# Performance work log

Measured on AMD Instinct MI355X. Metric: run time of the kernel, lower is better.

The kernel has to match this reference:

```python
import jax, jax.numpy as jnp
import numpy as np

HID = 128; H = 8; D = HID // H; L = 2; IN = 128; OUT = 32
ND = 20000; NF = 50000; E = 400000
SQRT_D = float(np.sqrt(D))
LN_EPS = 1e-5


def setup_inputs() -> dict:
    key = jax.random.key(0)
    ks = jax.random.split(key, 16)
    s = 1.0 / np.sqrt(HID)
    n = lambda k, sh, sc=1.0: jax.random.normal(k, sh, jnp.float32) * sc
    return dict(
        x_device=n(ks[0], (ND, IN)),
        x_feature=n(ks[1], (NF, IN)),
        e_df_src=jax.random.randint(ks[2], (E,), 0, ND),
        e_df_dst=jax.random.randint(ks[3], (E,), 0, NF),
        e_fd_src=jax.random.randint(ks[4], (E,), 0, NF),
        e_fd_dst=jax.random.randint(ks[5], (E,), 0, ND),
        W_dev_in=n(ks[6], (IN, HID), s), b_dev_in=jnp.zeros((HID,), jnp.float32),
        W_feat_in=n(ks[7], (IN, HID), s), b_feat_in=jnp.zeros((HID,), jnp.float32),
        Wk=n(ks[8], (L, 2, HID, HID), s), bk=jnp.zeros((L, 2, HID), jnp.float32),
        Wq=n(ks[9], (L, 2, HID, HID), s), bq=jnp.zeros((L, 2, HID), jnp.float32),
        Wv=n(ks[10], (L, 2, HID, HID), s), bv=jnp.zeros((L, 2, HID), jnp.float32),
        a_rel=n(ks[11], (L, 2, H, D, D), 1.0 / np.sqrt(D)),
        m_rel=n(ks[12], (L, 2, H, D, D), 1.0 / np.sqrt(D)),
        p_rel=jnp.ones((L, 2, H), jnp.float32),
        Wa=n(ks[13], (L, 2, HID, HID), s), ba=jnp.zeros((L, 2, HID), jnp.float32),
        skip=jnp.ones((L, 2), jnp.float32),
        ln_g=jnp.ones((L, 2, HID), jnp.float32), ln_b=jnp.zeros((L, 2, HID), jnp.float32),
        W_out=n(ks[14], (HID, OUT), s), b_out=jnp.zeros((OUT,), jnp.float32),
    )


def _layer_norm(x, g, b):
    m = x.mean(-1, keepdims=True)
    v = ((x - m) ** 2).mean(-1, keepdims=True)
    return (x - m) * jax.lax.rsqrt(v + LN_EPS) * g + b


def _edge_agg(q_dst, k_src, v_src, a_r, m_r, p_r, src, dst, n_dst):
    # per-edge-type relation transforms of source k/v: [N_src,H,D]
    kt = jnp.einsum('nhd,hde->nhe', k_src, a_r)
    vt = jnp.einsum('nhd,hde->nhe', v_src, m_r)
    # per-edge attention logits [E,H], scaled by relation prior
    logit = (q_dst[dst] * kt[src]).sum(-1) * p_r / SQRT_D
    # segment softmax over incoming edges of each dst node (per edge type)
    mx = jax.ops.segment_max(logit, dst, num_segments=n_dst)
    ex = jnp.exp(logit - mx[dst])
    sm = jax.ops.segment_sum(ex, dst, num_segments=n_dst)
    alpha = ex / (sm[dst] + 1e-16)
    # attention-weighted message scatter-sum -> [n_dst,H,D]
    return jax.ops.segment_sum(vt[src] * alpha[..., None], dst, num_segments=n_dst)


def _forward(x_device, x_feature, W_dev_in, b_dev_in, W_feat_in, b_feat_in,
             Wk, bk, Wq, bq, Wv, bv, a_rel, m_rel, p_rel, Wa, ba, skip,
             ln_g, ln_b, W_out, b_out, e_df_src, e_df_dst, e_fd_src, e_fd_dst):
    x_d = jax.nn.relu(x_device @ W_dev_in + b_dev_in)
    x_f = jax.nn.relu(x_feature @ W_feat_in + b_feat_in)
    for l in range(L):
        xs = (x_d, x_f)  # node-type 0 = device, 1 = feature
        k = [(xs[t] @ Wk[l, t] + bk[l, t]).reshape(-1, H, D) for t in range(2)]
        q = [(xs[t] @ Wq[l, t] + bq[l, t]).reshape(-1, H, D) for t in range(2)]
        v = [(xs[t] @ Wv[l, t] + bv[l, t]).reshape(-1, H, D) for t in range(2)]
        # edge type 0: device -> feature ; edge type 1: feature -> device
        agg_f = _edge_agg(q[1], k[0], v[0], a_rel[l, 0], m_rel[l, 0], p_rel[l, 0],
                          e_df_src, e_df_dst, NF)
        agg_d = _edge_agg(q[0], k[1], v[1], a_rel[l, 1], m_rel[l, 1], p_rel[l, 1],
                          e_fd_src, e_fd_dst, ND)
        new = []
        for t, agg in ((0, agg_d), (1, agg_f)):
            o = jax.nn.gelu(agg.reshape(-1, HID), approximate=False) @ Wa[l, t] + ba[l, t]
            sk = jax.nn.sigmoid(skip[l, t])
            o = sk * o + (1.0 - sk) * xs[t]              # HGTConv skip
            new.append(_layer_norm(xs[t] + o, ln_g[l, t], ln_b[l, t]))  # wrapper residual+LN (dropout=identity in eval)
        x_d, x_f = new
    return x_d @ W_out + b_out


def reference(x_device, x_feature, e_df_src, e_df_dst, e_fd_src, e_fd_dst,
              W_dev_in, b_dev_in, W_feat_in, b_feat_in, Wk, bk, Wq, bq, Wv, bv,
              a_rel, m_rel, p_rel, Wa, ba, skip, ln_g, ln_b, W_out, b_out):
    return _forward(x_device, x_feature, W_dev_in, b_dev_in, W_feat_in, b_feat_in,
                    Wk, bk, Wq, bq, Wv, bv, a_rel, m_rel, p_rel, Wa, ba, skip,
                    ln_g, ln_b, W_out, b_out, e_df_src, e_df_dst, e_fd_src, e_fd_dst)
```

## Files before the change

kernel.cpp:

```cpp
#include <hip/hip_runtime.h>
#include <math.h>

#define ND 20000
#define NF 50000
#define NE 400000
#define NT (NF + ND)
#define NBKT 256
#define BKTW 274

typedef __attribute__((ext_vector_type(8))) short short8;
typedef __attribute__((ext_vector_type(4))) float f32x4;
typedef __attribute__((ext_vector_type(2))) float f32x2;
typedef unsigned short us;
typedef unsigned char u8;

static __device__ __forceinline__ us f2bf(float f) {
    unsigned u = __builtin_bit_cast(unsigned, f);
    u += 0x7FFF + ((u >> 16) & 1);
    return (us)(u >> 16);
}
static __device__ __forceinline__ float bf2f(us h) {
    return __builtin_bit_cast(float, (unsigned)h << 16);
}
static __device__ __forceinline__ float bflo(unsigned u) {
    return __builtin_bit_cast(float, u << 16);
}
static __device__ __forceinline__ float bfhi(unsigned u) {
    return __builtin_bit_cast(float, u & 0xFFFF0000u);
}
static __device__ __forceinline__ float gelu_f(float x) {
    return 0.5f * x * (1.0f + erff(x * 0.70710678118654752f));
}

static __device__ __forceinline__ u8 f2fp8(float f) {
    unsigned u = __builtin_bit_cast(unsigned, f);
    unsigned s = (u >> 24) & 0x80u;
    unsigned a = u & 0x7FFFFFFFu;
    if (a >= 0x43E00000u) return (u8)(s | 0x7Eu);
    if (a < 0x3C800000u) {
        float af = __builtin_bit_cast(float, a);
        unsigned q = (unsigned)(af * 512.0f + 0.5f);
        return (u8)(s | q);
    }
    unsigned r = a + 0x7FFFFu + ((a >> 20) & 1u);
    unsigned e8 = (r >> 23) - 120u;
    unsigned m3 = (r >> 20) & 7u;
    return (u8)(s | (e8 << 3) | m3);
}

__global__ void k_hist_prep(const int* __restrict__ dA, const int* __restrict__ dB,
                            int* __restrict__ blockhist, int HB,
                            const float* __restrict__ W_dev_in, const float* __restrict__ W_feat_in,
                            const float* __restrict__ Wq, const float* __restrict__ Wk,
                            const float* __restrict__ Wv, const float* __restrict__ Wa,
                            const float* __restrict__ b_dev_in, const float* __restrict__ b_feat_in,
                            const float* __restrict__ bq, const float* __restrict__ bk,
                            const float* __restrict__ bv, const float* __restrict__ ba,
                            const float* __restrict__ a_rel, const float* __restrict__ m_rel,
                            const float* __restrict__ p_rel,
                            us* __restrict__ WT, float* __restrict__ B_all) {
    __shared__ int hist[NBKT];
    if ((int)blockIdx.x < HB) {
        hist[threadIdx.x] = 0;
        __syncthreads();
        int base_e = blockIdx.x * 4096;
        #pragma unroll
        for (int j = 0; j < 16; ++j) {
            int e = base_e + j * 256 + threadIdx.x;
            if (e < 2 * NE) {
                int g = (e < NE) ? dA[e] : (NF + dB[e - NE]);
                atomicAdd(&hist[g / BKTW], 1);
            }
        }
        __syncthreads();
        blockhist[blockIdx.x * NBKT + threadIdx.x] = hist[threadIdx.x];
        return;
    }
    int idx = (blockIdx.x - HB) * 256 + threadIdx.x;
    if (idx < 18 * 16384) {
        int k = idx & 127, c = (idx >> 7) & 127, id = idx >> 14;
        float val;
        if (id == 0) val = W_dev_in[k * 128 + c];
        else if (id == 1) val = W_feat_in[k * 128 + c];
        else if (id < 6) val = Wq[(id - 2) * 16384 + k * 128 + c];
        else if (id < 10) {
            int lt = id - 6, h = c >> 4, e = c & 15;
            const float* A = a_rel + (lt * 8 + h) * 256;
            const float* Ws = Wk + lt * 16384 + k * 128 + h * 16;
            float sm = 0.f;
            #pragma unroll
            for (int d = 0; d < 16; ++d) sm += Ws[d] * A[d * 16 + e];
            val = sm * p_rel[lt * 8 + h] * 0.25f;
        } else if (id < 14) {
            int lt = id - 10, h = c >> 4, e = c & 15;
            const float* A = m_rel + (lt * 8 + h) * 256;
            const float* Ws = Wv + lt * 16384 + k * 128 + h * 16;
            float sm = 0.f;
            #pragma unroll
            for (int d = 0; d < 16; ++d) sm += Ws[d] * A[d * 16 + e];
            val = sm;
        } else val = Wa[(id - 14) * 16384 + k * 128 + c];
        WT[(size_t)id * 16384 + (((c * 128 + k)) ^ ((c & 7) << 3))] = f2bf(val);
    } else {
        int j = idx - 18 * 16384;
        if (j >= 18 * 128) return;
        int c = j & 127, id = j >> 7;
        float v;
        if (id == 0) v = b_dev_in[c];
        else if (id == 1) v = b_feat_in[c];
        else if (id < 6) v = bq[(id - 2) * 128 + c];
        else if (id < 10) {
            int lt = id - 6, h = c >> 4, e = c & 15;
            const float* A = a_rel + (lt * 8 + h) * 256;
            const float* bs = bk + lt * 128 + h * 16;
            float sm = 0.f;
            #pragma unroll
            for (int d = 0; d < 16; ++d) sm += bs[d] * A[d * 16 + e];
            v = sm * p_rel[lt * 8 + h] * 0.25f;
        } else if (id < 14) {
            int lt = id - 10, h = c >> 4, e = c & 15;
            const float* A = m_rel + (lt * 8 + h) * 256;
            const float* bs = bv + lt * 128 + h * 16;
            float sm = 0.f;
            #pragma unroll
            for (int d = 0; d < 16; ++d) sm += bs[d] * A[d * 16 + e];
            v = sm;
        } else v = ba[(id - 14) * 128 + c];
        B_all[j] = v;
    }
}

__global__ void k_scanA(int* __restrict__ blockhist, int* __restrict__ totals, int HB) {
    __shared__ int sd[256];
    int b = blockIdx.x, t = threadIdx.x;
    int v = (t < HB) ? blockhist[t * NBKT + b] : 0;
    sd[t] = v; __syncthreads();
    for (int off = 1; off < 256; off <<= 1) {
        int add = (t >= off) ? sd[t - off] : 0;
        __syncthreads();
        sd[t] += add;
        __syncthreads();
    }
    if (t < HB) blockhist[t * NBKT + b] = sd[t] - v;
    if (t == 255) totals[b] = sd[255];
}

__global__ void k_scatter(const int* __restrict__ sA, const int* __restrict__ dA,
                          const int* __restrict__ sB, const int* __restrict__ dB,
                          const int* __restrict__ blockhist, const int* __restrict__ totals,
                          uint2* __restrict__ pairs) {
    __shared__ int lcur[NBKT];
    __shared__ int sdb[NBKT];
    int t = threadIdx.x;
    int tv = totals[t];
    sdb[t] = tv; __syncthreads();
    for (int off = 1; off < 256; off <<= 1) {
        int add = (t >= off) ? sdb[t - off] : 0;
        __syncthreads();
        sdb[t] += add;
        __syncthreads();
    }
    lcur[t] = (sdb[t] - tv) + blockhist[blockIdx.x * NBKT + t];
    __syncthreads();
    int base_e = blockIdx.x * 4096;
    #pragma unroll
    for (int j = 0; j < 16; ++j) {
        int e = base_e + j * 256 + t;
        if (e < 2 * NE) {
            int src, g;
            if (e < NE) { src = sA[e]; g = dA[e]; }
            else        { src = sB[e - NE]; g = NF + dB[e - NE]; }
            int pos = atomicAdd(&lcur[g / BKTW], 1);
            pairs[pos] = make_uint2((unsigned)src, (unsigned)g);
        }
    }
}

__global__ void k_bucket_csr(const uint2* __restrict__ pairs, const int* __restrict__ totals,
                             int* __restrict__ rs, int* __restrict__ esrc) {
    __shared__ int cnt[BKTW];
    __shared__ int excl[BKTW];
    __shared__ int sdb[NBKT];
    __shared__ int sde[NBKT];
    int b = blockIdx.x, t = threadIdx.x;
    int tv = totals[t];
    sdb[t] = tv; __syncthreads();
    for (int off = 1; off < 256; off <<= 1) {
        int add = (t >= off) ? sdb[t - off] : 0;
        __syncthreads();
        sdb[t] += add;
        __syncthreads();
    }
    sde[t] = sdb[t] - tv;
    __syncthreads();
    int start = sde[b], end = sdb[b];
    int g0 = b * BKTW;
    for (int i = t; i < BKTW; i += 256) cnt[i] = 0;
    __syncthreads();
    for (int i = start + t; i < end; i += 256)
        atomicAdd(&cnt[(int)pairs[i].y - g0], 1);
    __syncthreads();
    if (t < 64) {
        int lane = t;
        int vals[5]; int s = 0;
        #pragma unroll
        for (int j = 0; j < 5; ++j) {
            int i = lane * 5 + j;
            vals[j] = (i < BKTW) ? cnt[i] : 0;
            s += vals[j];
        }
        int incl = s;
        #pragma unroll
        for (int off = 1; off < 64; off <<= 1) {
            int n = __shfl_up(incl, off);
            if (lane >= off) incl += n;
        }
        int run = incl - s;
        #pragma unroll
        for (int j = 0; j < 5; ++j) {
            int i = lane * 5 + j;
            if (i < BKTW) excl[i] = run;
            run += vals[j];
        }
    }
    __syncthreads();
    int nloc = min(BKTW, NT - g0);
    for (int i = t; i < nloc; i += 256) rs[g0 + i] = start + excl[i];
    if (b == NBKT - 1 && t == 0) rs[NT] = sdb[255];
    __syncthreads();
    for (int i = start + t; i < end; i += 256) {
        uint2 p = pairs[i];
        int pos = start + atomicAdd(&excl[(int)p.y - g0], 1);
        esrc[pos] = (int)p.x;
    }
}

template<int MODE, int AF32, int RELU>
__global__ __launch_bounds__(256) void mfma_gemm2(
    const void* __restrict__ X0, const void* __restrict__ X1,
    const us* __restrict__ WT0, const float* __restrict__ Ball,
    us* __restrict__ Y0, us* __restrict__ Y1,
    int N0, int N1, int GB0, int widbase,
    us* __restrict__ K0, us* __restrict__ K1,
    u8* __restrict__ V0, u8* __restrict__ V1,
    const float* __restrict__ skipv, const float* __restrict__ lng,
    const float* __restrict__ lnb) {
    __shared__ us Wlds[16384];
    const int type = (blockIdx.x >= (unsigned)GB0) ? 1 : 0;
    const int bx = blockIdx.x - (type ? GB0 : 0);
    const int N = type ? N1 : N0;
    const void* Xv = type ? X1 : X0;
    const int NP = (MODE == 1) ? 3 : 1;

    const int lane = threadIdx.x & 63;
    const int wave = threadIdx.x >> 6;
    const int row_base = bx * 128 + wave * 32;
    const int l15 = lane & 15, lg = lane >> 4;
    const int kbase = lg * 8;

    {
        const char* gsrc = (const char*)(WT0 + (size_t)(widbase + type) * 16384)
                           + wave * 8192 + lane * 16;
        char* ldst = (char*)Wlds + wave * 8192;
        #pragma unroll
        for (int i = 0; i < 8; ++i) {
            __builtin_amdgcn_global_load_lds(
                (const __attribute__((address_space(1))) void*)(gsrc + i * 1024),
                (__attribute__((address_space(3))) void*)(ldst + i * 1024),
                16, 0, 0);
        }
    }

    short8 a[2][4];
    #pragma unroll
    for (int mf = 0; mf < 2; ++mf) {
        int r = row_base + mf * 16 + l15;
        r = r < N ? r : N - 1;
        if (AF32) {
            const float* Xf = (const float*)Xv + (size_t)r * 128;
            #pragma unroll
            for (int kf = 0; kf < 4; ++kf) {
                float4 lo = *(const float4*)(Xf + kf * 32 + kbase);
                float4 hi = *(const float4*)(Xf + kf * 32 + kbase + 4);
                short8 t;
                t[0] = (short)f2bf(lo.x); t[1] = (short)f2bf(lo.y);
                t[2] = (short)f2bf(lo.z); t[3] = (short)f2bf(lo.w);
                t[4] = (short)f2bf(hi.x); t[5] = (short)f2bf(hi.y);
                t[6] = (short)f2bf(hi.z); t[7] = (short)f2bf(hi.w);
                a[mf][kf] = t;
            }
        } else {
            const us* Xb = (const us*)Xv + (size_t)r * 128;
            #pragma unroll
            for (int kf = 0; kf < 4; ++kf)
                a[mf][kf] = *(const short8*)(Xb + kf * 32 + kbase);
        }
    }

    __syncthreads();

    const unsigned swz = (unsigned)((l15 & 7) << 4);

    for (int p = 0; p < NP; ++p) {
        const int wid = widbase + type + 4 * p;
        const float* bias = Ball + wid * 128;

        f32x4 acc[2][8];
        #pragma unroll
        for (int mf = 0; mf < 2; ++mf)
            #pragma unroll
            for (int cf = 0; cf < 8; ++cf) acc[mf][cf] = (f32x4){0.f, 0.f, 0.f, 0.f};

        #pragma unroll
        for (int cf = 0; cf < 8; ++cf) {
            const unsigned rowbyte = (unsigned)((cf * 16 + l15) * 256 + kbase * 2);
            #pragma unroll
            for (int kf = 0; kf < 4; ++kf) {
                short8 b = *(const short8*)((const char*)Wlds + ((rowbyte + kf * 64) ^ swz));
                acc[0][cf] = __builtin_amdgcn_mfma_f32_16x16x32_bf16(a[0][kf], b, acc[0][cf], 0, 0, 0);
                acc[1][cf] = __builtin_amdgcn_mfma_f32_16x16x32_bf16(a[1][kf], b, acc[1][cf], 0, 0, 0);
            }
        }

        if (MODE == 1 && p + 1 < NP) {
            __syncthreads();
            const char* gsrc = (const char*)(WT0 + (size_t)(widbase + type + 4 * (p + 1)) * 16384)
                               + wave * 8192 + lane * 16;
            char* ldst = (char*)Wlds + wave * 8192;
            #pragma unroll
            for (int i = 0; i < 8; ++i) {
                __builtin_amdgcn_global_load_lds(
                    (const __attribute__((address_space(1))) void*)(gsrc + i * 1024),
                    (__attribute__((address_space(3))) void*)(ldst + i * 1024),
                    16, 0, 0);
            }
        }

        float bval[8];
        #pragma unroll
        for (int cf = 0; cf < 8; ++cf) bval[cf] = bias[cf * 16 + l15];

        if (MODE == 2) {
            const int lt = widbase - 14 + type;
            float sk = 1.f / (1.f + __expf(-skipv[lt]));
            float gv[8], bv2[8];
            #pragma unroll
            for (int cf = 0; cf < 8; ++cf) {
                gv[cf]  = lng[(size_t)lt * 128 + cf * 16 + l15];
                bv2[cf] = lnb[(size_t)lt * 128 + cf * 16 + l15];
            }
            us* xw = type ? K1 : K0;
            #pragma unroll
            for (int mf = 0; mf < 2; ++mf)
                #pragma unroll
                for (int r = 0; r < 4; ++r) {
                    int grow = row_base + mf * 16 + lg * 4 + r;
                    if (grow >= N) continue;
                    float t[8];
                    float sum = 0.f;
                    #pragma unroll
                    for (int cf = 0; cf < 8; ++cf) {
                        float o = acc[mf][cf][r] + bval[cf];
                        float x = bf2f(xw[(size_t)grow * 128 + cf * 16 + l15]);
                        t[cf] = (2.f - sk) * x + sk * o;
                        sum += t[cf];
                    }
                    sum += __shfl_xor(sum, 1); sum += __shfl_xor(sum, 2);
                    sum += __shfl_xor(sum, 4); sum += __shfl_xor(sum, 8);
                    float mean = sum * (1.0f / 128.0f);
                    float vs = 0.f;
                    #pragma unroll
                    for (int cf = 0; cf < 8; ++cf) { t[cf] -= mean; vs += t[cf] * t[cf]; }
                    vs += __shfl_xor(vs, 1); vs += __shfl_xor(vs, 2);
                    vs += __shfl_xor(vs, 4); vs += __shfl_xor(vs, 8);
                    float inv = rsqrtf(vs * (1.0f / 128.0f) + 1e-5f);
                    #pragma unroll
                    for (int cf = 0; cf < 8; ++cf)
                        xw[(size_t)grow * 128 + cf * 16 + l15] = f2bf(t[cf] * inv * gv[cf] + bv2[cf]);
                }
        } else {
            #pragma unroll
            for (int mf = 0; mf < 2; ++mf)
                #pragma unroll
                for (int r = 0; r < 4; ++r) {
                    int grow = row_base + mf * 16 + lg * 4 + r;
                    if (grow >= N) continue;
                    #pragma unroll
                    for (int cf = 0; cf < 8; ++cf) {
                        float v = acc[mf][cf][r] + bval[cf];
                        if (RELU) v = fmaxf(v, 0.f);
                        int col = cf * 16 + l15;
                        if (MODE == 0 || p == 0) {
                            (type ? Y1 : Y0)[(size_t)grow * 128 + col] = f2bf(v);
                        } else if (p == 1) {
                            (type ? K1 : K0)[(size_t)grow * 128 + col] = f2bf(v);
                        } else {
                            (type ? V1 : V0)[(size_t)grow * 128 + col] = f2fp8(v);
                        }
                    }
                }
        }

        if (MODE == 1 && p + 1 < NP) __syncthreads();
    }
}

__global__ __launch_bounds__(256) void gemm_out_k(
    const us* __restrict__ X, const float* __restrict__ W,
    const float* __restrict__ bias, float* __restrict__ Y, int N) {
    __shared__ float Ws[128 * 32];
    __shared__ float Xs[8][128];
    const int tid = threadIdx.x;
    const int row0 = blockIdx.x * 8;
    #pragma unroll
    for (int it = 0; it < 16; ++it) Ws[it * 256 + tid] = W[it * 256 + tid];
    #pragma unroll
    for (int it = 0; it < 2; ++it) {
        int idx = it * 256 + tid;
        int rr = idx >> 6, kp = idx & 63;
        int gr = row0 + rr;
        unsigned u = (gr < N) ? *(const unsigned*)(X + (size_t)gr * 128 + kp * 2) : 0u;
        Xs[rr][kp * 2]     = bflo(u);
        Xs[rr][kp * 2 + 1] = bfhi(u);
    }
    __syncthreads();
    const int rr = tid >> 5, c = tid & 31;
    float acc = bias[c];
    #pragma unroll 8
    for (int k = 0; k < 128; ++k)
        acc = fmaf(Xs[rr][k], Ws[k * 32 + c], acc);
    int gr = row0 + rr;
    if (gr < N) Y[(size_t)gr * 32 + c] = acc;
}

#define EDGE_STEP(kc, vc, pidx)                                        \
    {                                                                  \
        float part = qv[0] * bflo(kc.x);                               \
        part = fmaf(qv[1], bfhi(kc.x), part);                          \
        part = fmaf(qv[2], bflo(kc.y), part);                          \
        part = fmaf(qv[3], bfhi(kc.y), part);                          \
        part = fmaf(qv[4], bflo(kc.z), part);                          \
        part = fmaf(qv[5], bfhi(kc.z), part);                          \
        part = fmaf(qv[6], bflo(kc.w), part);                          \
        part = fmaf(qv[7], bfhi(kc.w), part);                          \
        part += __shfl_xor(part, 1);                                   \
        float w = ((pidx) < p1) ? __expf(part) : 0.f;                  \
        s += w;                                                        \
        f32x2 v01 = __builtin_amdgcn_cvt_pk_f32_fp8((int)vc.x, false); \
        f32x2 v23 = __builtin_amdgcn_cvt_pk_f32_fp8((int)vc.x, true);  \
        f32x2 v45 = __builtin_amdgcn_cvt_pk_f32_fp8((int)vc.y, false); \
        f32x2 v67 = __builtin_amdgcn_cvt_pk_f32_fp8((int)vc.y, true);  \
        a[0] = fmaf(w, v01.x, a[0]);                                   \
        a[1] = fmaf(w, v01.y, a[1]);                                   \
        a[2] = fmaf(w, v23.x, a[2]);                                   \
        a[3] = fmaf(w, v23.y, a[3]);                                   \
        a[4] = fmaf(w, v45.x, a[4]);                                   \
        a[5] = fmaf(w, v45.y, a[5]);                                   \
        a[6] = fmaf(w, v67.x, a[6]);                                   \
        a[7] = fmaf(w, v67.y, a[7]);                                   \
    }

__global__ __launch_bounds__(256) void edge_agg6(
    const us* __restrict__ qf, const us* __restrict__ qd,
    const us* __restrict__ ktf, const us* __restrict__ ktd,
    const u8* __restrict__ v8f, const u8* __restrict__ v8d,
    const int* __restrict__ rs, const int* __restrict__ esrc,
    us* __restrict__ aggf, us* __restrict__ aggd) {
    int g = (blockIdx.x * 256 + threadIdx.x) >> 4;
    int li = threadIdx.x & 15;
    if (g >= NT) return;
    const us *q, *kt; const u8* v8; us* agg; int dst;
    if (g < NF) { dst = g;      q = qf; kt = ktd; v8 = v8d; agg = aggf; }
    else        { dst = g - NF; q = qd; kt = ktf; v8 = v8f; agg = aggd; }

    uint4 qb = *(const uint4*)(q + (size_t)dst * 128 + li * 8);
    float qv[8];
    qv[0] = bflo(qb.x); qv[1] = bfhi(qb.x);
    qv[2] = bflo(qb.y); qv[3] = bfhi(qb.y);
    qv[4] = bflo(qb.z); qv[5] = bfhi(qb.z);
    qv[6] = bflo(qb.w); qv[7] = bfhi(qb.w);

    const int p0 = rs[g], p1 = rs[g + 1];
    float s = 0.f;
    float a[8];
    #pragma unroll
    for (int j = 0; j < 8; ++j) a[j] = 0.f;

    const size_t loff = (size_t)li * 8;
    uint4 kA0, kA1, kB0, kB1;
    uint2 vA0, vA1, vB0, vB1;
    int sN0, sN1, sN2, sN3;

    if (p0 < p1) {
        const int last = p1 - 1;
        int s0 = esrc[p0], s1 = esrc[min(p0 + 1, last)];
        int s2 = esrc[min(p0 + 2, last)], s3 = esrc[min(p0 + 3, last)];
        kA0 = *(const uint4*)(kt + (size_t)s0 * 128 + loff);
        vA0 = *(const uint2*)(v8 + (size_t)s0 * 128 + loff);
        kA1 = *(const uint4*)(kt + (size_t)s1 * 128 + loff);
        vA1 = *(const uint2*)(v8 + (size_t)s1 * 128 + loff);
        kB0 = *(const uint4*)(kt + (size_t)s2 * 128 + loff);
        vB0 = *(const uint2*)(v8 + (size_t)s2 * 128 + loff);
        kB1 = *(const uint4*)(kt + (size_t)s3 * 128 + loff);
        vB1 = *(const uint2*)(v8 + (size_t)s3 * 128 + loff);
        sN0 = esrc[min(p0 + 4, last)];
        sN1 = esrc[min(p0 + 5, last)];
        sN2 = esrc[min(p0 + 6, last)];
        sN3 = esrc[min(p0 + 7, last)];

        for (int p = p0; p < p1; p += 4) {
            const int lastc = last;
            EDGE_STEP(kA0, vA0, p);
            EDGE_STEP(kA1, vA1, p + 1);
            kA0 = *(const uint4*)(kt + (size_t)sN0 * 128 + loff);
            vA0 = *(const uint2*)(v8 + (size_t)sN0 * 128 + loff);
            kA1 = *(const uint4*)(kt + (size_t)sN1 * 128 + loff);
            vA1 = *(const uint2*)(v8 + (size_t)sN1 * 128 + loff);
            sN0 = esrc[min(p + 8, lastc)];
            sN1 = esrc[min(p + 9, lastc)];
            EDGE_STEP(kB0, vB0, p + 2);
            EDGE_STEP(kB1, vB1, p + 3);
            kB0 = *(const uint4*)(kt + (size_t)sN2 * 128 + loff);
            vB0 = *(const uint2*)(v8 + (size_t)sN2 * 128 + loff);
            kB1 = *(const uint4*)(kt + (size_t)sN3 * 128 + loff);
            vB1 = *(const uint2*)(v8 + (size_t)sN3 * 128 + loff);
            sN2 = esrc[min(p + 10, lastc)];
            sN3 = esrc[min(p + 11, lastc)];
        }
    }

    float r = 1.0f / (s + 1e-16f);
    unsigned o[4];
    #pragma unroll
    for (int j = 0; j < 4; ++j) {
        us lo = f2bf(gelu_f(a[2 * j] * r));
        us hi = f2bf(gelu_f(a[2 * j + 1] * r));
        o[j] = (unsigned)lo | ((unsigned)hi << 16);
    }
    *(uint4*)(agg + (size_t)dst * 128 + li * 8) = make_uint4(o[0], o[1], o[2], o[3]);
}

extern "C" void kernel_launch(void* const* d_in, const int* in_sizes, int n_in,
                              void* d_out, int out_size, void* d_ws, size_t ws_size,
                              hipStream_t stream) {
    const float* x_device = (const float*)d_in[0];
    const float* x_feature = (const float*)d_in[1];
    const int* e_df_src = (const int*)d_in[2];
    const int* e_df_dst = (const int*)d_in[3];
    const int* e_fd_src = (const int*)d_in[4];
    const int* e_fd_dst = (const int*)d_in[5];
    const float* W_dev_in = (const float*)d_in[6];
    const float* b_dev_in = (const float*)d_in[7];
    const float* W_feat_in = (const float*)d_in[8];
    const float* b_feat_in = (const float*)d_in[9];
    const float* Wk = (const float*)d_in[10];
    const float* bk = (const float*)d_in[11];
    const float* Wq = (const float*)d_in[12];
    const float* bq = (const float*)d_in[13];
    const float* Wv = (const float*)d_in[14];
    const float* bv = (const float*)d_in[15];
    const float* a_rel = (const float*)d_in[16];
    const float* m_rel = (const float*)d_in[17];
    const float* p_rel = (const float*)d_in[18];
    const float* Wa = (const float*)d_in[19];
    const float* ba = (const float*)d_in[20];
    const float* skip = (const float*)d_in[21];
    const float* ln_g = (const float*)d_in[22];
    const float* ln_b = (const float*)d_in[23];
    const float* W_out = (const float*)d_in[24];
    const float* b_out = (const float*)d_in[25];

    char* ws = (char*)d_ws;
    size_t off = 0;
    auto alloc = [&](size_t bytes) -> void* {
        void* p = ws + off;
        off = (off + bytes + 255) & ~(size_t)255;
        return p;
    };
    us* xd     = (us*)alloc((size_t)ND * 128 * 2);
    us* xf     = (us*)alloc((size_t)NF * 128 * 2);
    us* q_d    = (us*)alloc((size_t)ND * 128 * 2);
    us* q_f    = (us*)alloc((size_t)NF * 128 * 2);
    us* kt_d   = (us*)alloc((size_t)ND * 128 * 2);
    us* kt_f   = (us*)alloc((size_t)NF * 128 * 2);
    u8* v8_d   = (u8*)alloc((size_t)ND * 128);
    u8* v8_f   = (u8*)alloc((size_t)NF * 128);
    us* agg_d  = (us*)alloc((size_t)ND * 128 * 2);
    us* agg_f  = (us*)alloc((size_t)NF * 128 * 2);
    us* WT     = (us*)alloc((size_t)18 * 16384 * 2);
    float* B_all = (float*)alloc(18 * 128 * 4);
    int* rs     = (int*)alloc((size_t)(NT + 1) * 4);
    int* esrc   = (int*)alloc((size_t)(2 * NE + 8) * 4);
    uint2* pairs = (uint2*)alloc((size_t)2 * NE * 8);
    int* blockhist = (int*)alloc((size_t)200 * NBKT * 4);
    int* totals = (int*)alloc(NBKT * 4);

    const int HB = (2 * NE + 4095) / 4096;
    const int PB = (18 * 16384 + 18 * 128 + 255) / 256;

    k_hist_prep<<<HB + PB, 256, 0, stream>>>(
        e_df_dst, e_fd_dst, blockhist, HB,
        W_dev_in, W_feat_in, Wq, Wk, Wv, Wa,
        b_dev_in, b_feat_in, bq, bk, bv, ba,
        a_rel, m_rel, p_rel, WT, B_all);
    k_scanA<<<NBKT, 256, 0, stream>>>(blockhist, totals, HB);
    k_scatter<<<HB, 256, 0, stream>>>(e_df_src, e_df_dst, e_fd_src, e_fd_dst,
                                      blockhist, totals, pairs);
    k_bucket_csr<<<NBKT, 256, 0, stream>>>(pairs, totals, rs, esrc);

    const int GBD = (ND + 127) / 128, GBF = (NF + 127) / 128;

    mfma_gemm2<0, 1, 1><<<GBD + GBF, 256, 0, stream>>>(
        x_device, x_feature, WT, B_all, xd, xf, ND, NF, GBD, 0,
        nullptr, nullptr, nullptr, nullptr, nullptr, nullptr, nullptr);

    for (int l = 0; l < 2; ++l) {
        mfma_gemm2<1, 0, 0><<<GBD + GBF, 256, 0, stream>>>(
            xd, xf, WT, B_all, q_d, q_f, ND, NF, GBD, 2 + l * 2,
            kt_d, kt_f, v8_d, v8_f, nullptr, nullptr, nullptr);

        edge_agg6<<<((NT * 16) + 255) / 256, 256, 0, stream>>>(
            q_f, q_d, kt_f, kt_d, v8_f, v8_d, rs, esrc, agg_f, agg_d);

        mfma_gemm2<2, 0, 0><<<GBD + GBF, 256, 0, stream>>>(
            agg_d, agg_f, WT, B_all, nullptr, nullptr, ND, NF, GBD, 14 + l * 2,
            xd, xf, nullptr, nullptr, skip, ln_g, ln_b);
    }

    gemm_out_k<<<(ND + 7) / 8, 256, 0, stream>>>(xd, W_out, b_out, (float*)d_out, ND);
}
```

Before: 257.1 us.

## Store transformed K in fp8 interleaved with V for single gathered load

The projection GEMM now writes the relation-transformed keys as fp8 instead of bf16, interleaved byte-wise with the fp8 values into one 256-byte row per node. The edge aggregation kernel then gathers one 16-byte load per edge per lane instead of a 16-byte K load plus an 8-byte V load, and unpacks K and V together with packed fp8 conversions. This cuts gathered bytes per edge and halves the number of scattered memory requests. In exchange, attention logits are computed from lower-precision keys, which adds numerical error to the softmax, and the interleaved byte stores in the GEMM epilogue are narrower and less coalesced.

After: 257.2 us. Within noise of the previous version (+0.1%).

```diff
diff --git a/kernel.cpp b/kernel.cpp
--- a/kernel.cpp
+++ b/kernel.cpp
@@ -242,7 +242,7 @@
     us* __restrict__ Y0, us* __restrict__ Y1,
     int N0, int N1, int GB0, int widbase,
     us* __restrict__ K0, us* __restrict__ K1,
-    u8* __restrict__ V0, u8* __restrict__ V1,
+    u8* __restrict__ KV0, u8* __restrict__ KV1,
     const float* __restrict__ skipv, const float* __restrict__ lng,
     const float* __restrict__ lnb) {
     __shared__ us Wlds[16384];
@@ -392,10 +392,8 @@
                         int col = cf * 16 + l15;
                         if (MODE == 0 || p == 0) {
                             (type ? Y1 : Y0)[(size_t)grow * 128 + col] = f2bf(v);
-                        } else if (p == 1) {
-                            (type ? K1 : K0)[(size_t)grow * 128 + col] = f2bf(v);
                         } else {
-                            (type ? V1 : V0)[(size_t)grow * 128 + col] = f2fp8(v);
+                            (type ? KV1 : KV0)[(size_t)grow * 256 + col * 2 + (p - 1)] = f2fp8(v);
                         }
                     }
                 }
@@ -433,45 +431,48 @@
     if (gr < N) Y[(size_t)gr * 32 + c] = acc;
 }
 
-#define EDGE_STEP(kc, vc, pidx)                                        \
-    {                                                                  \
-        float part = qv[0] * bflo(kc.x);                               \
-        part = fmaf(qv[1], bfhi(kc.x), part);                          \
-        part = fmaf(qv[2], bflo(kc.y), part);                          \
-        part = fmaf(qv[3], bfhi(kc.y), part);                          \
-        part = fmaf(qv[4], bflo(kc.z), part);                          \
-        part = fmaf(qv[5], bfhi(kc.z), part);                          \
-        part = fmaf(qv[6], bflo(kc.w), part);                          \
-        part = fmaf(qv[7], bfhi(kc.w), part);                          \
-        part += __shfl_xor(part, 1);                                   \
-        float w = ((pidx) < p1) ? __expf(part) : 0.f;                  \
-        s += w;                                                        \
-        f32x2 v01 = __builtin_amdgcn_cvt_pk_f32_fp8((int)vc.x, false); \
-        f32x2 v23 = __builtin_amdgcn_cvt_pk_f32_fp8((int)vc.x, true);  \
-        f32x2 v45 = __builtin_amdgcn_cvt_pk_f32_fp8((int)vc.y, false); \
-        f32x2 v67 = __builtin_amdgcn_cvt_pk_f32_fp8((int)vc.y, true);  \
-        a[0] = fmaf(w, v01.x, a[0]);                                   \
-        a[1] = fmaf(w, v01.y, a[1]);                                   \
-        a[2] = fmaf(w, v23.x, a[2]);                                   \
-        a[3] = fmaf(w, v23.y, a[3]);                                   \
-        a[4] = fmaf(w, v45.x, a[4]);                                   \
-        a[5] = fmaf(w, v45.y, a[5]);                                   \
-        a[6] = fmaf(w, v67.x, a[6]);                                   \
-        a[7] = fmaf(w, v67.y, a[7]);                                   \
-    }
-
-__global__ __launch_bounds__(256) void edge_agg6(
+#define EDGE_STEP(kvc, pidx)                                              \
+    {                                                                     \
+        f32x2 d0 = __builtin_amdgcn_cvt_pk_f32_fp8((int)kvc.x, false);    \
+        f32x2 d1 = __builtin_amdgcn_cvt_pk_f32_fp8((int)kvc.x, true);     \
+        f32x2 d2 = __builtin_amdgcn_cvt_pk_f32_fp8((int)kvc.y, false);    \
+        f32x2 d3 = __builtin_amdgcn_cvt_pk_f32_fp8((int)kvc.y, true);     \
+        f32x2 d4 = __builtin_amdgcn_cvt_pk_f32_fp8((int)kvc.z, false);    \
+        f32x2 d5 = __builtin_amdgcn_cvt_pk_f32_fp8((int)kvc.z, true);     \
+        f32x2 d6 = __builtin_amdgcn_cvt_pk_f32_fp8((int)kvc.w, false);    \
+        f32x2 d7 = __builtin_amdgcn_cvt_pk_f32_fp8((int)kvc.w, true);     \
+        float part = qv[0] * d0.x;                                        \
+        part = fmaf(qv[1], d1.x, part);                                   \
+        part = fmaf(qv[2], d2.x, part);                                   \
+        part = fmaf(qv[3], d3.x, part);                                   \
+        part = fmaf(qv[4], d4.x, part);                                   \
+        part = fmaf(qv[5], d5.x, part);                                   \
+        part = fmaf(qv[6], d6.x, part);                                   \
+        part = fmaf(qv[7], d7.x, part);                                   \
+        part += __shfl_xor(part, 1);                                      \
+        float w = ((pidx) < p1) ? __expf(part) : 0.f;                     \
+        s += w;                                                           \
+        a[0] = fmaf(w, d0.y, a[0]);                                       \
+        a[1] = fmaf(w, d1.y, a[1]);                                       \
+        a[2] = fmaf(w, d2.y, a[2]);                                       \
+        a[3] = fmaf(w, d3.y, a[3]);                                       \
+        a[4] = fmaf(w, d4.y, a[4]);                                       \
+        a[5] = fmaf(w, d5.y, a[5]);                                       \
+        a[6] = fmaf(w, d6.y, a[6]);                                       \
+        a[7] = fmaf(w, d7.y, a[7]);                                       \
+    }
+
+__global__ __launch_bounds__(256) void edge_agg7(
     const us* __restrict__ qf, const us* __restrict__ qd,
-    const us* __restrict__ ktf, const us* __restrict__ ktd,
-    const u8* __restrict__ v8f, const u8* __restrict__ v8d,
+    const u8* __restrict__ kv8f, const u8* __restrict__ kv8d,
     const int* __restrict__ rs, const int* __restrict__ esrc,
     us* __restrict__ aggf, us* __restrict__ aggd) {
     int g = (blockIdx.x * 256 + threadIdx.x) >> 4;
     int li = threadIdx.x & 15;
     if (g >= NT) return;
-    const us *q, *kt; const u8* v8; us* agg; int dst;
-    if (g < NF) { dst = g;      q = qf; kt = ktd; v8 = v8d; agg = aggf; }
-    else        { dst = g - NF; q = qd; kt = ktf; v8 = v8f; agg = aggd; }
+    const us* q; const u8* kv8; us* agg; int dst;
+    if (g < NF) { dst = g;      q = qf; kv8 = kv8d; agg = aggf; }
+    else        { dst = g - NF; q = qd; kv8 = kv8f; agg = aggd; }
 
     uint4 qb = *(const uint4*)(q + (size_t)dst * 128 + li * 8);
     float qv[8];
@@ -486,23 +487,18 @@
     #pragma unroll
     for (int j = 0; j < 8; ++j) a[j] = 0.f;
 
-    const size_t loff = (size_t)li * 8;
-    uint4 kA0, kA1, kB0, kB1;
-    uint2 vA0, vA1, vB0, vB1;
+    const size_t loff = (size_t)li * 16;
+    uint4 kvA0, kvA1, kvB0, kvB1;
     int sN0, sN1, sN2, sN3;
 
     if (p0 < p1) {
         const int last = p1 - 1;
         int s0 = esrc[p0], s1 = esrc[min(p0 + 1, last)];
         int s2 = esrc[min(p0 + 2, last)], s3 = esrc[min(p0 + 3, last)];
-        kA0 = *(const uint4*)(kt + (size_t)s0 * 128 + loff);
-        vA0 = *(const uint2*)(v8 + (size_t)s0 * 128 + loff);
-        kA1 = *(const uint4*)(kt + (size_t)s1 * 128 + loff);
-        vA1 = *(const uint2*)(v8 + (size_t)s1 * 128 + loff);
-        kB0 = *(const uint4*)(kt + (size_t)s2 * 128 + loff);
-        vB0 = *(const uint2*)(v8 + (size_t)s2 * 128 + loff);
-        kB1 = *(const uint4*)(kt + (size_t)s3 * 128 + loff);
-        vB1 = *(const uint2*)(v8 + (size_t)s3 * 128 + loff);
+        kvA0 = *(const uint4*)(kv8 + (size_t)s0 * 256 + loff);
+        kvA1 = *(const uint4*)(kv8 + (size_t)s1 * 256 + loff);
+        kvB0 = *(const uint4*)(kv8 + (size_t)s2 * 256 + loff);
+        kvB1 = *(const uint4*)(kv8 + (size_t)s3 * 256 + loff);
         sN0 = esrc[min(p0 + 4, last)];
         sN1 = esrc[min(p0 + 5, last)];
         sN2 = esrc[min(p0 + 6, last)];
@@ -510,20 +506,16 @@
 
         for (int p = p0; p < p1; p += 4) {
             const int lastc = last;
-            EDGE_STEP(kA0, vA0, p);
-            EDGE_STEP(kA1, vA1, p + 1);
-            kA0 = *(const uint4*)(kt + (size_t)sN0 * 128 + loff);
-            vA0 = *(const uint2*)(v8 + (size_t)sN0 * 128 + loff);
-            kA1 = *(const uint4*)(kt + (size_t)sN1 * 128 + loff);
-            vA1 = *(const uint2*)(v8 + (size_t)sN1 * 128 + loff);
+            EDGE_STEP(kvA0, p);
+            EDGE_STEP(kvA1, p + 1);
+            kvA0 = *(const uint4*)(kv8 + (size_t)sN0 * 256 + loff);
+            kvA1 = *(const uint4*)(kv8 + (size_t)sN1 * 256 + loff);
             sN0 = esrc[min(p + 8, lastc)];
             sN1 = esrc[min(p + 9, lastc)];
-            EDGE_STEP(kB0, vB0, p + 2);
-            EDGE_STEP(kB1, vB1, p + 3);
-            kB0 = *(const uint4*)(kt + (size_t)sN2 * 128 + loff);
-            vB0 = *(const uint2*)(v8 + (size_t)sN2 * 128 + loff);
-            kB1 = *(const uint4*)(kt + (size_t)sN3 * 128 + loff);
-            vB1 = *(const uint2*)(v8 + (size_t)sN3 * 128 + loff);
+            EDGE_STEP(kvB0, p + 2);
+            EDGE_STEP(kvB1, p + 3);
+            kvB0 = *(const uint4*)(kv8 + (size_t)sN2 * 256 + loff);
+            kvB1 = *(const uint4*)(kv8 + (size_t)sN3 * 256 + loff);
             sN2 = esrc[min(p + 10, lastc)];
             sN3 = esrc[min(p + 11, lastc)];
         }
@@ -581,10 +573,8 @@
     us* xf     = (us*)alloc((size_t)NF * 128 * 2);
     us* q_d    = (us*)alloc((size_t)ND * 128 * 2);
     us* q_f    = (us*)alloc((size_t)NF * 128 * 2);
-    us* kt_d   = (us*)alloc((size_t)ND * 128 * 2);
-    us* kt_f   = (us*)alloc((size_t)NF * 128 * 2);
-    u8* v8_d   = (u8*)alloc((size_t)ND * 128);
-    u8* v8_f   = (u8*)alloc((size_t)NF * 128);
+    u8* kv8_d  = (u8*)alloc((size_t)ND * 256);
+    u8* kv8_f  = (u8*)alloc((size_t)NF * 256);
     us* agg_d  = (us*)alloc((size_t)ND * 128 * 2);
     us* agg_f  = (us*)alloc((size_t)NF * 128 * 2);
     us* WT     = (us*)alloc((size_t)18 * 16384 * 2);
@@ -617,10 +607,10 @@
     for (int l = 0; l < 2; ++l) {
         mfma_gemm2<1, 0, 0><<<GBD + GBF, 256, 0, stream>>>(
             xd, xf, WT, B_all, q_d, q_f, ND, NF, GBD, 2 + l * 2,
-            kt_d, kt_f, v8_d, v8_f, nullptr, nullptr, nullptr);
-
-        edge_agg6<<<((NT * 16) + 255) / 256, 256, 0, stream>>>(
-            q_f, q_d, kt_f, kt_d, v8_f, v8_d, rs, esrc, agg_f, agg_d);
+            nullptr, nullptr, kv8_d, kv8_f, nullptr, nullptr, nullptr);
+
+        edge_agg7<<<((NT * 16) + 255) / 256, 256, 0, stream>>>(
+            q_f, q_d, kv8_f, kv8_d, rs, esrc, agg_f, agg_d);
 
         mfma_gemm2<2, 0, 0><<<GBD + GBF, 256, 0, stream>>>(
             agg_d, agg_f, WT, B_all, nullptr, nullptr, ND, NF, GBD, 14 + l * 2,
```
